# Performance work log

Measured on AMD Instinct MI355X. Metric: run time of the kernel, lower is better.

## Reference

```python
import jax, jax.numpy as jnp
import numpy as np

DIM = 2048
NUM_EXPERTS = 64
TOPK = 8
ROUTE_SCALE = 1.0


def setup_inputs() -> dict:
    key = jax.random.key(0)
    kx, kw = jax.random.split(key)
    x = jax.random.normal(kx, (16384, DIM), dtype=jnp.float32)
    # xavier_uniform_ for weight of shape (num_experts, dim)
    limit = float(np.sqrt(6.0 / (NUM_EXPERTS + DIM)))
    weight = jax.random.uniform(kw, (NUM_EXPERTS, DIM), dtype=jnp.float32,
                                minval=-limit, maxval=limit)
    bias = jnp.zeros((NUM_EXPERTS,), dtype=jnp.float32)
    return {"x": x, "weight": weight, "bias": bias}


def reference(x, weight, bias):
    # logits: (N, E) = x @ weight.T + bias
    logits = jnp.einsum('nd,ed->ne', x, weight) + bias
    probs = jax.nn.softmax(logits * ROUTE_SCALE, axis=-1)
    topk_vals, topk_idx = jax.lax.top_k(probs, TOPK)  # (N, topk) each
    # dense gate: scatter topk_vals into (N, num_experts)
    N = x.shape[0]
    dense_gate = jnp.zeros((N, NUM_EXPERTS), dtype=probs.dtype)
    rows = jnp.arange(N)[:, None]
    dense_gate = dense_gate.at[rows, topk_idx].set(topk_vals)
    return topk_vals, topk_idx, dense_gate
```

## Files before the change

### kernel.cpp

```cpp
#include <hip/hip_runtime.h>
#include <math.h>

#pragma clang fp contract(off)


#define NROWS 16384
#define DIM   2048
#define NE    64
#define MARGIN 1e-4f
#define MAXCAND 12
#define WS_WOFF (512 * 1024)

typedef float f32x4 __attribute__((ext_vector_type(4)));
typedef short s16x8 __attribute__((ext_vector_type(8)));

__device__ __forceinline__ void ld16_lds(const float* g, void* l) {
  __builtin_amdgcn_global_load_lds((const __attribute__((address_space(1))) void*)g,
                                   (__attribute__((address_space(3))) void*)l, 16, 0, 0);
}
__device__ __forceinline__ unsigned short bf16_rne(float f) {
  unsigned u = __builtin_bit_cast(unsigned, f);
  u += 0x7FFFu + ((u >> 16) & 1u);
  return (unsigned short)(u >> 16);
}
__device__ __forceinline__ float bf16f(unsigned short h) {
  return __builtin_bit_cast(float, (unsigned)h << 16);
}
__device__ __forceinline__ void cvt8(const f32x4 a, const f32x4 b, s16x8* hi, s16x8* lo) {
#pragma unroll
  for (int j = 0; j < 4; ++j) {
    unsigned short h = bf16_rne(a[j]);
    (*hi)[j] = (short)h; (*lo)[j] = (short)bf16_rne(a[j] - bf16f(h));
  }
#pragma unroll
  for (int j = 0; j < 4; ++j) {
    unsigned short h = bf16_rne(b[j]);
    (*hi)[4 + j] = (short)h; (*lo)[4 + j] = (short)bf16_rne(b[j] - bf16f(h));
  }
}

__global__ __launch_bounds__(256, 8)
void w_split(const float* __restrict__ w, unsigned short* __restrict__ whf,
             unsigned short* __restrict__ wlf) {
  const int i = blockIdx.x * 256 + threadIdx.x;
  const int e = i >> 11, k = i & 2047;
  float v = w[i];
  unsigned short h = bf16_rne(v);
  unsigned short lo = bf16_rne(v - bf16f(h));
  const int n = e >> 4, col = e & 15;
  const int kt = k >> 5, j = k & 31;
  const int lane = col | ((j >> 3) << 4);
  const size_t off = (((size_t)(kt << 2) + n) * 64 + lane) * 8 + (j & 7);
  whf[off] = h; wlf[off] = lo;
}

template <bool USE_WS>
__global__ __launch_bounds__(512, 4)
void mfma_logits(const float* __restrict__ x, const float* __restrict__ w,
                 const float* __restrict__ bias, float* __restrict__ lg,
                 const unsigned short* __restrict__ whf,
                 const unsigned short* __restrict__ wlf)
{
  __shared__ float part[8][64][33];

  const int t = threadIdx.x;
  const int wv = t >> 6, lane = t & 63;
  const int rowBase = blockIdx.x << 5;
  const int frow = lane & 15;
  const int fk   = (lane >> 4) << 3;
  const size_t q0 = (size_t)wv * 256;

  const float* xb0 = x + (size_t)(rowBase + frow) * DIM + q0 + fk;
  const float* xb1 = xb0 + (size_t)16 * DIM;
  const float* wb = w + (size_t)frow * DIM + q0 + fk;
  const int ktg0 = wv << 3;

  f32x4 acc[2][4];
#pragma unroll
  for (int m = 0; m < 2; ++m)
#pragma unroll
    for (int n = 0; n < 4; ++n) acc[m][n] = (f32x4)(0.f);

#pragma unroll 2
  for (int kt = 0; kt < 8; ++kt) {
    const int ko = kt << 5;
    s16x8 ah0, al0, ah1, al1;
    {
      f32x4 a0 = *(const f32x4*)(xb0 + ko);
      f32x4 a1 = *(const f32x4*)(xb0 + ko + 4);
      cvt8(a0, a1, &ah0, &al0);
      f32x4 c0 = *(const f32x4*)(xb1 + ko);
      f32x4 c1 = *(const f32x4*)(xb1 + ko + 4);
      cvt8(c0, c1, &ah1, &al1);
    }
#pragma unroll
    for (int n = 0; n < 4; ++n) {
      s16x8 bh, bl;
      if constexpr (USE_WS) {
        const size_t foff = (((size_t)((ktg0 + kt) << 2) + n) * 64 + lane) * 8;
        bh = *(const s16x8*)(whf + foff);
        bl = *(const s16x8*)(wlf + foff);
      } else {
        const float* wp = wb + (size_t)(n << 4) * DIM + ko;
        f32x4 b0 = *(const f32x4*)(wp);
        f32x4 b1 = *(const f32x4*)(wp + 4);
        cvt8(b0, b1, &bh, &bl);
      }
      acc[0][n] = __builtin_amdgcn_mfma_f32_16x16x32_bf16(al0, bh, acc[0][n], 0, 0, 0);
      acc[0][n] = __builtin_amdgcn_mfma_f32_16x16x32_bf16(ah0, bl, acc[0][n], 0, 0, 0);
      acc[0][n] = __builtin_amdgcn_mfma_f32_16x16x32_bf16(ah0, bh, acc[0][n], 0, 0, 0);
      acc[1][n] = __builtin_amdgcn_mfma_f32_16x16x32_bf16(al1, bh, acc[1][n], 0, 0, 0);
      acc[1][n] = __builtin_amdgcn_mfma_f32_16x16x32_bf16(ah1, bl, acc[1][n], 0, 0, 0);
      acc[1][n] = __builtin_amdgcn_mfma_f32_16x16x32_bf16(ah1, bh, acc[1][n], 0, 0, 0);
    }
  }

#pragma unroll
  for (int m = 0; m < 2; ++m)
#pragma unroll
    for (int n = 0; n < 4; ++n)
#pragma unroll
      for (int r = 0; r < 4; ++r)
        part[wv][(n << 4) + (lane & 15)][(m << 4) + ((lane >> 4) << 2) + r] = acc[m][n][r];
  __syncthreads();

#pragma unroll
  for (int i = t; i < 2048; i += 512) {
    const int row = i >> 6, col = i & 63;
    float v = ((part[0][col][row] + part[1][col][row])
             + (part[2][col][row] + part[3][col][row]))
            + ((part[4][col][row] + part[5][col][row])
             + (part[6][col][row] + part[7][col][row]));
    lg[(size_t)(rowBase + row) * NE + col] = v + bias[col];
  }
}

__global__ __launch_bounds__(256, 4)
void finish_kernel(float* __restrict__ gate, float* __restrict__ out_vals,
                   float* __restrict__ out_idx, int* __restrict__ flags, int maxf)
{
  const int t    = threadIdx.x;
  const int row  = blockIdx.x * 4 + (t >> 6);
  const int lane = t & 63;

  float l = gate[(size_t)row * NE + lane];

  float m = l;
#pragma unroll
  for (int d = 32; d >= 1; d >>= 1) m = fmaxf(m, __shfl_xor(m, d));
  float pe = expf(l - m);
  float s = pe;
#pragma unroll
  for (int d = 32; d >= 1; d >>= 1) s = s + __shfl_xor(s, d);
  float p = pe / s;

  float cur = l;
  float sval[9]; int sidx[9];
  unsigned long long used8 = 0;
#pragma unroll
  for (int k = 0; k < 9; ++k) {
    float v = cur; int i = lane;
#pragma unroll
    for (int d = 1; d < 64; d <<= 1) {
      float ov = __shfl_xor(v, d);
      int   oi = __shfl_xor(i, d);
      bool take = (ov > v) || (ov == v && oi < i);
      v = take ? ov : v;
      i = take ? oi : i;
    }
    sval[k] = v; sidx[k] = i;
    if (k < 8) {
      used8 |= 1ull << i;
      if (lane == i) cur = -INFINITY;
    }
  }

  float myv = 0.f, myi = 0.f;
#pragma unroll
  for (int k = 0; k < 8; ++k) {
    float pv = __shfl(p, sidx[k]);
    if (lane == k) { myv = pv; myi = (float)sidx[k]; }
  }
  if (lane < 8) {
    out_vals[(size_t)row * 8 + lane] = myv;
    out_idx [(size_t)row * 8 + lane] = myi;
  }

  gate[(size_t)row * NE + lane] = ((used8 >> lane) & 1ull) ? p : 0.0f;

  float ming = INFINITY;
#pragma unroll
  for (int k = 1; k < 9; ++k) ming = fminf(ming, sval[k - 1] - sval[k]);
  if (ming < MARGIN && maxf > 0) {
    unsigned long long cmask = __ballot(l >= sval[7] - MARGIN);
    int n = __popcll(cmask);
    if (n <= MAXCAND) {
      int slot = 0;
      if (lane == 0) slot = atomicAdd(flags, 1);
      slot = __shfl(slot, 0);
      if (slot < maxf) {
        int* rec = flags + 4 + slot * 32;
        if (lane == 0) { rec[0] = row; rec[1] = n; }
        if ((cmask >> lane) & 1ull) {
          int pos = __popcll(cmask & ((1ull << lane) - 1ull));
          rec[2 + pos] = lane;
          ((float*)(rec + 14))[pos] = p;
        }
      }
    }
  }
}

__global__ __launch_bounds__(64, 1)
void exact_fix(const float* __restrict__ x, const float* __restrict__ w,
               const float* __restrict__ bias, const int* __restrict__ flags,
               int maxf, float* __restrict__ out_vals, float* __restrict__ out_idx,
               float* __restrict__ gate)
{
  __shared__ float xs_[DIM];
  __shared__ float wl_[MAXCAND * DIM];
  __shared__ float exl[MAXCAND];

  int count = flags[0]; if (count > maxf) count = maxf;
  const int lane = threadIdx.x;

  for (int recI = blockIdx.x; recI < count; recI += (int)gridDim.x) {
    const int* rec = flags + 4 + recI * 32;
    const int row = rec[0], n = rec[1];

#pragma unroll
    for (int i = 0; i < 8; ++i)
      ld16_lds(x + (size_t)row * DIM + i * 256 + lane * 4, &xs_[i * 256 + lane * 4]);
    for (int c = 0; c < n; ++c)
#pragma unroll
      for (int i = 0; i < 8; ++i)
        ld16_lds(w + (size_t)rec[2 + c] * DIM + i * 256 + lane * 4,
                 &wl_[c * DIM + i * 256 + lane * 4]);
    asm volatile("s_waitcnt vmcnt(0)" ::: "memory");
    __builtin_amdgcn_s_barrier();

    const int c = lane >> 2, jj = lane & 3;
    const int cw = (c < n) ? c : 0;
    const float* wrow = &wl_[cw * DIM];
    float a = 0.f;
#pragma unroll 4
    for (int b = 0; b < 128; ++b) {
      const int k = (b << 4) + jj;
      a = a + xs_[k + 12] * wrow[k + 12];
      a = a + xs_[k + 8]  * wrow[k + 8];
      a = a + xs_[k + 4]  * wrow[k + 4];
      a = a + xs_[k]      * wrow[k];
    }
    float o1 = __shfl_xor(a, 1);
    float s01 = a + o1;
    float o2 = __shfl_xor(s01, 2);
    float tot = (s01 + o2) + bias[rec[2 + cw]];
    if (jj == 0 && c < n) exl[c] = tot;
    __syncthreads();

    if (lane == 0) {
      unsigned used = 0;
      const float* cp = (const float*)(rec + 14);
      for (int k = 0; k < 8; ++k) {
        float best = -INFINITY; int bi = 0;
        for (int c2 = 0; c2 < n; ++c2) {
          bool ok = (((used >> c2) & 1u) == 0u) && (exl[c2] > best);
          best = ok ? exl[c2] : best;
          bi   = ok ? c2      : bi;
        }
        used |= 1u << bi;
        out_vals[(size_t)row * 8 + k] = cp[bi];
        out_idx [(size_t)row * 8 + k] = (float)rec[2 + bi];
      }
      for (int c2 = 0; c2 < n; ++c2)
        gate[(size_t)row * NE + rec[2 + c2]] = ((used >> c2) & 1u) ? cp[c2] : 0.f;
    }
    __syncthreads();
  }
}

extern "C" void kernel_launch(void* const* d_in, const int* in_sizes, int n_in,
                              void* d_out, int out_size, void* d_ws, size_t ws_size,
                              hipStream_t stream) {
  const float* x    = (const float*)d_in[0];
  const float* w    = (const float*)d_in[1];
  const float* bias = (const float*)d_in[2];
  float* out   = (float*)d_out;
  float* vals  = out;
  float* idx   = out + (size_t)NROWS * 8;
  float* dense = out + (size_t)NROWS * 16;
  (void)in_sizes; (void)n_in; (void)out_size;

  const bool use_ws_w = ws_size >= WS_WOFF + (size_t)NE * DIM * 4;
  int maxf = 0;
  if (ws_size >= 16 + 32 * 4) {
    size_t cap = (ws_size / 4 - 4) / 32;
    if (cap > 2048) cap = 2048;
    if (use_ws_w) { size_t cap2 = (WS_WOFF / 4 - 4) / 32; if (cap > cap2) cap = cap2; }
    maxf = (int)cap;
  }
  int* flags = (int*)d_ws;
  unsigned short* whf = (unsigned short*)((char*)d_ws + WS_WOFF);
  unsigned short* wlf = whf + (size_t)NE * DIM;

  if (use_ws_w) {
    w_split<<<dim3(NE * DIM / 256), dim3(256), 0, stream>>>(w, whf, wlf);
    mfma_logits<true><<<dim3(NROWS / 32), dim3(512), 0, stream>>>(x, w, bias, dense, whf, wlf);
  } else {
    mfma_logits<false><<<dim3(NROWS / 32), dim3(512), 0, stream>>>(x, w, bias, dense, whf, wlf);
  }
  if (maxf > 0) hipMemsetAsync(d_ws, 0, 16, stream);
  finish_kernel<<<dim3(NROWS / 4), dim3(256), 0, stream>>>(dense, vals, idx, flags, maxf);
  if (maxf > 0)
    exact_fix<<<dim3(128), dim3(64), 0, stream>>>(x, w, bias, flags, maxf, vals, idx, dense);
}
```

Before: 81.65 us.

## Double rows per logits block to reuse weight fragments; zero flags via kernel

The logits GEMM block now covers 64 rows instead of 32. Each loaded bf16 hi/lo weight fragment feeds four row tiles of MFMAs instead of two, which halves per-row weight traffic from L2. To fit the larger accumulator set, launch bounds drop to 2 blocks per CU, the k-loop is no longer unrolled, and the LDS reduction epilogue runs in two phases that reuse the same shared buffer. Separately, the 16-byte hipMemsetAsync of the flag area is replaced by a tiny kernel that zeroes only flags[0], cutting memset overhead but clearing fewer bytes than before. The grid halves to 256 blocks, so there is less parallelism and less latency hiding.

```diff
diff --git a/kernel.cpp b/kernel.cpp
--- a/kernel.cpp
+++ b/kernel.cpp
@@ -54,8 +54,12 @@
   whf[off] = h; wlf[off] = lo;
 }
 
+__global__ void zero_flags(int* __restrict__ flags) {
+  if (threadIdx.x == 0) flags[0] = 0;
+}
+
 template <bool USE_WS>
-__global__ __launch_bounds__(512, 4)
+__global__ __launch_bounds__(512, 2)
 void mfma_logits(const float* __restrict__ x, const float* __restrict__ w,
                  const float* __restrict__ bias, float* __restrict__ lg,
                  const unsigned short* __restrict__ whf,
@@ -65,33 +69,38 @@
 
   const int t = threadIdx.x;
   const int wv = t >> 6, lane = t & 63;
-  const int rowBase = blockIdx.x << 5;
+  const int rowBase = blockIdx.x << 6;
   const int frow = lane & 15;
   const int fk   = (lane >> 4) << 3;
   const size_t q0 = (size_t)wv * 256;
 
   const float* xb0 = x + (size_t)(rowBase + frow) * DIM + q0 + fk;
   const float* xb1 = xb0 + (size_t)16 * DIM;
+  const float* xb2 = xb0 + (size_t)32 * DIM;
+  const float* xb3 = xb0 + (size_t)48 * DIM;
   const float* wb = w + (size_t)frow * DIM + q0 + fk;
   const int ktg0 = wv << 3;
 
-  f32x4 acc[2][4];
-#pragma unroll
-  for (int m = 0; m < 2; ++m)
+  f32x4 acc[4][4];
+#pragma unroll
+  for (int m = 0; m < 4; ++m)
 #pragma unroll
     for (int n = 0; n < 4; ++n) acc[m][n] = (f32x4)(0.f);
 
-#pragma unroll 2
+#pragma unroll 1
   for (int kt = 0; kt < 8; ++kt) {
     const int ko = kt << 5;
-    s16x8 ah0, al0, ah1, al1;
+    s16x8 ah[4], al[4];
     {
-      f32x4 a0 = *(const f32x4*)(xb0 + ko);
-      f32x4 a1 = *(const f32x4*)(xb0 + ko + 4);
-      cvt8(a0, a1, &ah0, &al0);
-      f32x4 c0 = *(const f32x4*)(xb1 + ko);
-      f32x4 c1 = *(const f32x4*)(xb1 + ko + 4);
-      cvt8(c0, c1, &ah1, &al1);
+      f32x4 a0, a1;
+      a0 = *(const f32x4*)(xb0 + ko); a1 = *(const f32x4*)(xb0 + ko + 4);
+      cvt8(a0, a1, &ah[0], &al[0]);
+      a0 = *(const f32x4*)(xb1 + ko); a1 = *(const f32x4*)(xb1 + ko + 4);
+      cvt8(a0, a1, &ah[1], &al[1]);
+      a0 = *(const f32x4*)(xb2 + ko); a1 = *(const f32x4*)(xb2 + ko + 4);
+      cvt8(a0, a1, &ah[2], &al[2]);
+      a0 = *(const f32x4*)(xb3 + ko); a1 = *(const f32x4*)(xb3 + ko + 4);
+      cvt8(a0, a1, &ah[3], &al[3]);
     }
 #pragma unroll
     for (int n = 0; n < 4; ++n) {
@@ -106,32 +115,37 @@
         f32x4 b1 = *(const f32x4*)(wp + 4);
         cvt8(b0, b1, &bh, &bl);
       }
-      acc[0][n] = __builtin_amdgcn_mfma_f32_16x16x32_bf16(al0, bh, acc[0][n], 0, 0, 0);
-      acc[0][n] = __builtin_amdgcn_mfma_f32_16x16x32_bf16(ah0, bl, acc[0][n], 0, 0, 0);
-      acc[0][n] = __builtin_amdgcn_mfma_f32_16x16x32_bf16(ah0, bh, acc[0][n], 0, 0, 0);
-      acc[1][n] = __builtin_amdgcn_mfma_f32_16x16x32_bf16(al1, bh, acc[1][n], 0, 0, 0);
-      acc[1][n] = __builtin_amdgcn_mfma_f32_16x16x32_bf16(ah1, bl, acc[1][n], 0, 0, 0);
-      acc[1][n] = __builtin_amdgcn_mfma_f32_16x16x32_bf16(ah1, bh, acc[1][n], 0, 0, 0);
-    }
-  }
-
-#pragma unroll
-  for (int m = 0; m < 2; ++m)
-#pragma unroll
-    for (int n = 0; n < 4; ++n)
-#pragma unroll
-      for (int r = 0; r < 4; ++r)
-        part[wv][(n << 4) + (lane & 15)][(m << 4) + ((lane >> 4) << 2) + r] = acc[m][n][r];
-  __syncthreads();
-
-#pragma unroll
-  for (int i = t; i < 2048; i += 512) {
-    const int row = i >> 6, col = i & 63;
-    float v = ((part[0][col][row] + part[1][col][row])
-             + (part[2][col][row] + part[3][col][row]))
-            + ((part[4][col][row] + part[5][col][row])
-             + (part[6][col][row] + part[7][col][row]));
-    lg[(size_t)(rowBase + row) * NE + col] = v + bias[col];
+#pragma unroll
+      for (int m = 0; m < 4; ++m) {
+        acc[m][n] = __builtin_amdgcn_mfma_f32_16x16x32_bf16(al[m], bh, acc[m][n], 0, 0, 0);
+        acc[m][n] = __builtin_amdgcn_mfma_f32_16x16x32_bf16(ah[m], bl, acc[m][n], 0, 0, 0);
+        acc[m][n] = __builtin_amdgcn_mfma_f32_16x16x32_bf16(ah[m], bh, acc[m][n], 0, 0, 0);
+      }
+    }
+  }
+
+#pragma unroll
+  for (int ph = 0; ph < 2; ++ph) {
+    if (ph) __syncthreads();
+#pragma unroll
+    for (int mm = 0; mm < 2; ++mm) {
+      const int m = (ph << 1) + mm;
+#pragma unroll
+      for (int n = 0; n < 4; ++n)
+#pragma unroll
+        for (int r = 0; r < 4; ++r)
+          part[wv][(n << 4) + (lane & 15)][(mm << 4) + ((lane >> 4) << 2) + r] = acc[m][n][r];
+    }
+    __syncthreads();
+#pragma unroll
+    for (int i = t; i < 2048; i += 512) {
+      const int row = i >> 6, col = i & 63;
+      float v = ((part[0][col][row] + part[1][col][row])
+               + (part[2][col][row] + part[3][col][row]))
+              + ((part[4][col][row] + part[5][col][row])
+               + (part[6][col][row] + part[7][col][row]));
+      lg[(size_t)(rowBase + (ph << 5) + row) * NE + col] = v + bias[col];
+    }
   }
 }
 
@@ -305,11 +319,11 @@
 
   if (use_ws_w) {
     w_split<<<dim3(NE * DIM / 256), dim3(256), 0, stream>>>(w, whf, wlf);
-    mfma_logits<true><<<dim3(NROWS / 32), dim3(512), 0, stream>>>(x, w, bias, dense, whf, wlf);
+    mfma_logits<true><<<dim3(NROWS / 64), dim3(512), 0, stream>>>(x, w, bias, dense, whf, wlf);
   } else {
-    mfma_logits<false><<<dim3(NROWS / 32), dim3(512), 0, stream>>>(x, w, bias, dense, whf, wlf);
-  }
-  if (maxf > 0) hipMemsetAsync(d_ws, 0, 16, stream);
+    mfma_logits<false><<<dim3(NROWS / 64), dim3(512), 0, stream>>>(x, w, bias, dense, whf, wlf);
+  }
+  if (maxf > 0) zero_flags<<<dim3(1), dim3(64), 0, stream>>>(flags);
   finish_kernel<<<dim3(NROWS / 4), dim3(256), 0, stream>>>(dense, vals, idx, flags, maxf);
   if (maxf > 0)
     exact_fix<<<dim3(128), dim3(64), 0, stream>>>(x, w, bias, flags, maxf, vals, idx, dense);
```

After: 91.39 us. +11.9%, slower.
